# Kernel optimization log

Hardware: AMD Instinct MI355X
Metric: run time of the kernel (lower is better)

## Reference

```python
import jax, jax.numpy as jnp
import numpy as np

B, N, C = 4, 1024, 768
H = 12
HD = C // H  # 64
SCALE = HD ** -0.5


def setup_inputs() -> dict:
    key = jax.random.key(0)
    ks = jax.random.split(key, 8)
    s = lambda fan: 1.0 / np.sqrt(fan)
    return {
        "inputs": jax.random.normal(ks[0], (B, N, C), jnp.float32),
        "w_qkv": jax.random.normal(ks[1], (C, 3 * C), jnp.float32) * s(C),
        "w_l": jax.random.normal(ks[2], (H, H), jnp.float32) * s(H),
        "b_l": jnp.zeros((H,), jnp.float32),
        "w_w": jax.random.normal(ks[3], (H, H), jnp.float32) * s(H),
        "b_w": jnp.zeros((H,), jnp.float32),
        "w_proj": jax.random.normal(ks[4], (C, C), jnp.float32) * s(C),
        "b_proj": jnp.zeros((C,), jnp.float32),
    }


def reference(inputs, w_qkv, w_l, b_l, w_w, b_w, w_proj, b_proj):
    b, n, c = inputs.shape
    qkv = inputs @ w_qkv                      # (B,N,3C), no bias (use_att_bias=False)
    qkv = qkv.reshape(b, n, 3, H, HD)
    qkv = jnp.transpose(qkv, (2, 0, 3, 1, 4))  # (3,B,H,N,HD)
    q = qkv[0] * SCALE
    k = qkv[1]
    v = qkv[2]
    att = jnp.einsum("bhqd,bhkd->bhqk", q, k)            # (B,H,N,N)
    # pre-softmax talking-heads mix over head axis
    att = jnp.einsum("bhqk,hg->bgqk", att, w_l) + b_l[None, :, None, None]
    att = jax.nn.softmax(att, axis=-1)
    # post-softmax talking-heads mix
    att = jnp.einsum("bhqk,hg->bgqk", att, w_w) + b_w[None, :, None, None]
    x = jnp.einsum("bhqk,bhkd->bqhd", att, v).reshape(b, n, c)
    return x @ w_proj + b_proj
```

## Files before the change

kernel.cpp:

```cpp
#include <hip/hip_runtime.h>


#define Bsz   4
#define Nseq  1024
#define Cdim  768
#define Hn    12
#define HDim  64

typedef __attribute__((ext_vector_type(4))) float    f32x4;
typedef __attribute__((ext_vector_type(2))) float    f32x2;
typedef __attribute__((ext_vector_type(8))) _Float16 f16x8;
typedef __attribute__((ext_vector_type(4))) _Float16 f16x4;

#define MFMA_F16(A, B, C) __builtin_amdgcn_mfma_f32_16x16x32_f16(A, B, C, 0, 0, 0)

__global__ __launch_bounds__(256) void cvt_f32_f16(
    const float* __restrict__ in, _Float16* __restrict__ out)
{
  const size_t i = (size_t)(blockIdx.x * 256 + threadIdx.x) * 4;
  float4 v = *(const float4*)(in + i);
  f16x4 o;
  o[0] = (_Float16)v.x; o[1] = (_Float16)v.y;
  o[2] = (_Float16)v.z; o[3] = (_Float16)v.w;
  *(f16x4*)(out + i) = o;
}

__global__ __launch_bounds__(256) void transpose_cvt(
    const float* __restrict__ in, _Float16* __restrict__ out, int R, int C)
{
  __shared__ float T[64][65];
  const int c0 = blockIdx.x * 64, r0 = blockIdx.y * 64;
  const int lr = threadIdx.x >> 4, lc = (threadIdx.x & 15) * 4;
#pragma unroll
  for (int i = 0; i < 4; ++i) {
    float4 v = *(const float4*)(in + (size_t)(r0 + lr + i*16) * C + c0 + lc);
    T[lr+i*16][lc+0] = v.x; T[lr+i*16][lc+1] = v.y;
    T[lr+i*16][lc+2] = v.z; T[lr+i*16][lc+3] = v.w;
  }
  __syncthreads();
#pragma unroll
  for (int i = 0; i < 4; ++i) {
    const int orow = lr + i*16;
    f16x4 o;
#pragma unroll
    for (int j = 0; j < 4; ++j) o[j] = (_Float16)T[lc+j][orow];
    *(f16x4*)(out + (size_t)(c0 + orow) * R + r0 + lc) = o;
  }
}

__global__ __launch_bounds__(256, 2) void gemm_f16(
    const _Float16* __restrict__ A, const _Float16* __restrict__ Bt,
    const float* __restrict__ bias, _Float16* __restrict__ C16,
    float* __restrict__ C32, int M, int N, int K)
{
  __shared__ _Float16 sA[2][4][512];
  __shared__ _Float16 sB[2][4][512];
  const int tid = threadIdx.x;
  const int w = tid >> 6, lane = tid & 63;
  const int m0 = blockIdx.y * 128, n0 = blockIdx.x * 128;
  const int frow = lane & 15, fk8 = lane >> 4;

  f32x4 acc[4][4];
#pragma unroll
  for (int i = 0; i < 4; ++i)
#pragma unroll
    for (int j = 0; j < 4; ++j) acc[i][j] = (f32x4)0.f;

  const _Float16* gsrc = (w < 2)
      ? A  + (size_t)(m0 + w*64 + frow) * K + fk8 * 8
      : Bt + (size_t)(n0 + (w - 2)*64 + frow) * K + fk8 * 8;

  for (int kt = 0; kt < K; kt += 32) {
    f16x8 st[4];
#pragma unroll
    for (int j = 0; j < 4; ++j)
      st[j] = *(const f16x8*)(gsrc + kt + (size_t)j * 16 * K);
    __syncthreads();
    if (w < 2) {
#pragma unroll
      for (int j = 0; j < 4; ++j) *(f16x8*)&sA[w][j][lane*8] = st[j];
    } else {
#pragma unroll
      for (int j = 0; j < 4; ++j) *(f16x8*)&sB[w-2][j][lane*8] = st[j];
    }
    __syncthreads();
    f16x8 af[4], bf[4];
#pragma unroll
    for (int mi = 0; mi < 4; ++mi) af[mi] = *(const f16x8*)&sA[w & 1][mi][lane*8];
#pragma unroll
    for (int ni = 0; ni < 4; ++ni) bf[ni] = *(const f16x8*)&sB[w >> 1][ni][lane*8];
#pragma unroll
    for (int mi = 0; mi < 4; ++mi)
#pragma unroll
      for (int ni = 0; ni < 4; ++ni)
        acc[mi][ni] = MFMA_F16(af[mi], bf[ni], acc[mi][ni]);
  }

  const int m0w = m0 + (w & 1) * 64, n0w = n0 + (w >> 1) * 64;
#pragma unroll
  for (int mi = 0; mi < 4; ++mi)
#pragma unroll
    for (int ni = 0; ni < 4; ++ni) {
      const int n = n0w + ni*16 + (lane & 15);
#pragma unroll
      for (int r = 0; r < 4; ++r) {
        const int m = m0w + mi*16 + (lane >> 4)*4 + r;
        if (C16) C16[(size_t)m * N + n] = (_Float16)acc[mi][ni][r];
        else     C32[(size_t)m * N + n] = acc[mi][ni][r] + bias[n];
      }
    }
}

__global__ __launch_bounds__(256, 2) void gemm_s16(
    const _Float16* __restrict__ qkv16, _Float16* __restrict__ S)
{
  __shared__ _Float16 sA[2][4][512];
  __shared__ _Float16 sB[2][4][512];
  const int tid = threadIdx.x;
  const int w = tid >> 6, lane = tid & 63;
  const int m0 = blockIdx.y * 128, n0 = blockIdx.x * 128;
  const int frow = lane & 15, fk8 = lane >> 4;
  const int bh = blockIdx.z;
  const int b = bh / Hn, h = bh % Hn;

  const _Float16* Abase = qkv16 + (size_t)(b * Nseq) * (3*Cdim) + h * HDim;
  const _Float16* Bbase = Abase + Cdim;

  f32x4 acc[4][4];
#pragma unroll
  for (int i = 0; i < 4; ++i)
#pragma unroll
    for (int j = 0; j < 4; ++j) acc[i][j] = (f32x4)0.f;

  const _Float16* gsrc = (w < 2)
      ? Abase + (size_t)(m0 + w*64 + frow) * (3*Cdim) + fk8 * 8
      : Bbase + (size_t)(n0 + (w - 2)*64 + frow) * (3*Cdim) + fk8 * 8;

#pragma unroll
  for (int kt = 0; kt < HDim; kt += 32) {
    f16x8 st[4];
#pragma unroll
    for (int j = 0; j < 4; ++j)
      st[j] = *(const f16x8*)(gsrc + kt + (size_t)j * 16 * (3*Cdim));
    __syncthreads();
    if (w < 2) {
#pragma unroll
      for (int j = 0; j < 4; ++j) *(f16x8*)&sA[w][j][lane*8] = st[j];
    } else {
#pragma unroll
      for (int j = 0; j < 4; ++j) *(f16x8*)&sB[w-2][j][lane*8] = st[j];
    }
    __syncthreads();
    f16x8 af[4], bf[4];
#pragma unroll
    for (int mi = 0; mi < 4; ++mi) af[mi] = *(const f16x8*)&sA[w & 1][mi][lane*8];
#pragma unroll
    for (int ni = 0; ni < 4; ++ni) bf[ni] = *(const f16x8*)&sB[w >> 1][ni][lane*8];
#pragma unroll
    for (int mi = 0; mi < 4; ++mi)
#pragma unroll
      for (int ni = 0; ni < 4; ++ni)
        acc[mi][ni] = MFMA_F16(af[mi], bf[ni], acc[mi][ni]);
  }

  _Float16* out = S + ((size_t)bh << 20);
  const int m0w = m0 + (w & 1) * 64, n0w = n0 + (w >> 1) * 64;
#pragma unroll
  for (int mi = 0; mi < 4; ++mi)
#pragma unroll
    for (int ni = 0; ni < 4; ++ni) {
      const int n = n0w + ni*16 + (lane & 15);
#pragma unroll
      for (int r = 0; r < 4; ++r) {
        const int m = m0w + mi*16 + (lane >> 4)*4 + r;
        out[(size_t)m * Nseq + n] = (_Float16)acc[mi][ni][r];
      }
    }
}

__global__ __launch_bounds__(256) void mixexp2_k(
    _Float16* __restrict__ S, const float* __restrict__ w_l,
    const float* __restrict__ w_w, const float* __restrict__ b_w)
{
  __shared__ __attribute__((aligned(16))) float wl_s[144];
  __shared__ __attribute__((aligned(16))) float ww_s[144];
  __shared__ float bw_s[12];
  const int tid = threadIdx.x;
  if (tid < 144) { wl_s[tid] = w_l[tid] * 0.125f; ww_s[tid] = w_w[tid]; }
  if (tid < 12)  bw_s[tid] = b_w[tid];
  __syncthreads();

  const int b    = blockIdx.x >> 8;
  const int qg   = blockIdx.x & 255;
  const int w    = tid >> 6;
  const int lane = tid & 63;
  const int q    = qg * 4 + w;
  const int ks   = lane * 16;
  _Float16* base = S + ((size_t)(b*Hn) << 20) + ((size_t)q << 10) + ks;

  f16x8 sv[12][2];
#pragma unroll
  for (int h = 0; h < 12; ++h) {
    sv[h][0] = *(const f16x8*)(base + ((size_t)h << 20));
    sv[h][1] = *(const f16x8*)(base + ((size_t)h << 20) + 8);
  }

  float dacc[12];
#pragma unroll
  for (int g = 0; g < 12; ++g) dacc[g] = 0.f;

#pragma unroll
  for (int bl = 0; bl < 2; ++bl) {
#pragma unroll
    for (int kp = 0; kp < 4; ++kp) {
      const int k0 = kp * 2;
      f32x2 L[12];
#pragma unroll
      for (int g = 0; g < 12; ++g) L[g] = (f32x2)0.f;
#pragma unroll
      for (int h = 0; h < 12; ++h) {
        f32x2 s2;
        s2.x = (float)sv[h][bl][k0];
        s2.y = (float)sv[h][bl][k0+1];
#pragma unroll
        for (int g = 0; g < 12; ++g)
          L[g] += s2 * wl_s[h*12 + g];
      }
#pragma unroll
      for (int g = 0; g < 12; ++g) {
        const _Float16 p0 = (_Float16)__expf(L[g].x - 6.0f);
        const _Float16 p1 = (_Float16)__expf(L[g].y - 6.0f);
        sv[g][bl][k0]   = p0;
        sv[g][bl][k0+1] = p1;
        dacc[g] += (float)p0 + (float)p1;
      }
    }
  }

#pragma unroll
  for (int g = 0; g < 12; ++g) {
    float v = dacc[g];
    v += __shfl_xor(v, 1, 64);
    v += __shfl_xor(v, 2, 64);
    v += __shfl_xor(v, 4, 64);
    v += __shfl_xor(v, 8, 64);
    v += __shfl_xor(v, 16, 64);
    v += __shfl_xor(v, 32, 64);
    dacc[g] = 1.0f / v;
  }

#pragma unroll
  for (int bl = 0; bl < 2; ++bl) {
#pragma unroll
    for (int kp = 0; kp < 4; ++kp) {
      const int k0 = kp * 2;
      f32x2 pr[12];
#pragma unroll
      for (int g = 0; g < 12; ++g) {
        f32x2 t;
        t.x = (float)sv[g][bl][k0];
        t.y = (float)sv[g][bl][k0+1];
        pr[g] = t * dacc[g];
      }
      f32x2 att[12];
#pragma unroll
      for (int g2 = 0; g2 < 12; ++g2) att[g2] = (f32x2)bw_s[g2];
#pragma unroll
      for (int g = 0; g < 12; ++g) {
#pragma unroll
        for (int g2 = 0; g2 < 12; ++g2)
          att[g2] += pr[g] * ww_s[g*12 + g2];
      }
#pragma unroll
      for (int g2 = 0; g2 < 12; ++g2) {
        sv[g2][bl][k0]   = (_Float16)att[g2].x;
        sv[g2][bl][k0+1] = (_Float16)att[g2].y;
      }
    }
  }

#pragma unroll
  for (int g2 = 0; g2 < 12; ++g2) {
    *(f16x8*)(base + ((size_t)g2 << 20))     = sv[g2][0];
    *(f16x8*)(base + ((size_t)g2 << 20) + 8) = sv[g2][1];
  }
}

__global__ __launch_bounds__(256) void prep_v(
    const _Float16* __restrict__ qkv16, _Float16* __restrict__ Vt)
{
  __shared__ float vt[64][65];
  const int id = blockIdx.x;
  const int nt = id & 15;
  const int h  = (id >> 4) % Hn;
  const int b  = id / (16 * Hn);
  const int n0 = nt * 64;
  const int tid = threadIdx.x;
  const int row = tid >> 2;
  const int c0  = (tid & 3) * 16;

  const _Float16* src = qkv16 + (size_t)(b*Nseq + n0 + row) * (3*Cdim) + 2*Cdim + h*HDim + c0;
  f16x8 v0 = *(const f16x8*)src;
  f16x8 v1 = *(const f16x8*)(src + 8);
#pragma unroll
  for (int j = 0; j < 8; ++j) {
    vt[c0+j][row]   = (float)v0[j];
    vt[c0+8+j][row] = (float)v1[j];
  }
  __syncthreads();
  f16x8 o0, o1;
#pragma unroll
  for (int j = 0; j < 8; ++j) {
    o0[j] = (_Float16)vt[row][c0+j];
    o1[j] = (_Float16)vt[row][c0+8+j];
  }
  _Float16* dst = Vt + (size_t)((b*Hn + h)*HDim + row) * Nseq + n0 + c0;
  *(f16x8*)dst = o0;
  *(f16x8*)(dst + 8) = o1;
}

__global__ __launch_bounds__(256, 2) void gemm_pv(
    const _Float16* __restrict__ P, const _Float16* __restrict__ Vt,
    _Float16* __restrict__ x16)
{
  __shared__ _Float16 sA[2][4][512];
  __shared__ _Float16 sB[4][512];
  const int tid = threadIdx.x;
  const int w = tid >> 6, lane = tid & 63;
  const int m0 = blockIdx.y * 128;
  const int bh = blockIdx.z;
  const int b = bh / Hn, g2 = bh % Hn;
  const int frow = lane & 15, fk8 = lane >> 4;

  const _Float16* Abase = P + ((size_t)bh << 20);
  const _Float16* Bbase = Vt + (size_t)(bh * HDim) * Nseq;

  f32x4 acc[4][2];
#pragma unroll
  for (int i = 0; i < 4; ++i)
#pragma unroll
    for (int j = 0; j < 2; ++j) acc[i][j] = (f32x4)0.f;

  const _Float16* gsrc = (w < 2)
      ? Abase + (size_t)(m0 + w*64 + frow) * Nseq + fk8 * 8
      : Bbase + (size_t)frow * Nseq + fk8 * 8;

  for (int kt = 0; kt < Nseq; kt += 32) {
    f16x8 st[4];
    if (w <= 2) {
#pragma unroll
      for (int j = 0; j < 4; ++j)
        st[j] = *(const f16x8*)(gsrc + kt + (size_t)j * 16 * Nseq);
    }
    __syncthreads();
    if (w < 2) {
#pragma unroll
      for (int j = 0; j < 4; ++j) *(f16x8*)&sA[w][j][lane*8] = st[j];
    } else if (w == 2) {
#pragma unroll
      for (int j = 0; j < 4; ++j) *(f16x8*)&sB[j][lane*8] = st[j];
    }
    __syncthreads();
    f16x8 af[4], bf[2];
#pragma unroll
    for (int mi = 0; mi < 4; ++mi) af[mi] = *(const f16x8*)&sA[w & 1][mi][lane*8];
#pragma unroll
    for (int ni = 0; ni < 2; ++ni) bf[ni] = *(const f16x8*)&sB[(w >> 1)*2 + ni][lane*8];
#pragma unroll
    for (int mi = 0; mi < 4; ++mi)
#pragma unroll
      for (int ni = 0; ni < 2; ++ni)
        acc[mi][ni] = MFMA_F16(af[mi], bf[ni], acc[mi][ni]);
  }

  const int m0w = m0 + (w & 1) * 64, n0w = (w >> 1) * 32;
#pragma unroll
  for (int mi = 0; mi < 4; ++mi)
#pragma unroll
    for (int ni = 0; ni < 2; ++ni) {
      const int n = n0w + ni*16 + (lane & 15);
#pragma unroll
      for (int r = 0; r < 4; ++r) {
        const int m = m0w + mi*16 + (lane >> 4)*4 + r;
        x16[(size_t)(b*Nseq + m) * Cdim + g2*HDim + n] = (_Float16)acc[mi][ni][r];
      }
    }
}

__global__ __launch_bounds__(256, 2) void dsum_k(
    const _Float16* __restrict__ qkv16, const float* __restrict__ w_l,
    float* __restrict__ dpart)
{
  __shared__ __attribute__((aligned(16))) float wl_s[144];
  __shared__ float dred[4][16][12];
  const int tid = threadIdx.x;
  const int w = tid >> 6, lane = tid & 63;
  const int col = lane & 15, grp = lane >> 4;
  const int ch = blockIdx.x & 7;
  const int qt = (blockIdx.x >> 3) & 63;
  const int b  = blockIdx.x >> 9;
  const int q0 = qt << 4;

  if (tid < 144) wl_s[tid] = w_l[tid] * 0.125f;

  f16x8 qf[12][2];
  {
    const _Float16* qrow = qkv16 + (size_t)(b*Nseq + q0 + col) * (3*Cdim) + grp*8;
#pragma unroll
    for (int h = 0; h < 12; ++h) {
      qf[h][0] = *(const f16x8*)(qrow + h*HDim);
      qf[h][1] = *(const f16x8*)(qrow + h*HDim + 32);
    }
  }
  __syncthreads();

  float dacc[4][12];
#pragma unroll
  for (int r = 0; r < 4; ++r)
#pragma unroll
    for (int g = 0; g < 12; ++g) dacc[r][g] = 0.f;

#pragma unroll
  for (int kg = 0; kg < 2; ++kg) {
    const int key = ch*128 + kg*64 + w*16 + col;
    const _Float16* krow = qkv16 + (size_t)(b*Nseq + key) * (3*Cdim) + Cdim + grp*8;
    f32x4 S[12];
#pragma unroll
    for (int h = 0; h < 12; ++h) {
      f16x8 b0 = *(const f16x8*)(krow + h*HDim);
      f16x8 b1 = *(const f16x8*)(krow + h*HDim + 32);
      f32x4 s = (f32x4)0.f;
      s = MFMA_F16(qf[h][0], b0, s);
      S[h] = MFMA_F16(qf[h][1], b1, s);
    }
#pragma unroll
    for (int r = 0; r < 4; ++r) {
      float L[12];
#pragma unroll
      for (int g = 0; g < 12; ++g) L[g] = 0.f;
#pragma unroll
      for (int h = 0; h < 12; ++h) {
        const float s = S[h][r];
        const f32x4 w0 = *(const f32x4*)&wl_s[h*12];
        const f32x4 w1 = *(const f32x4*)&wl_s[h*12+4];
        const f32x4 w2 = *(const f32x4*)&wl_s[h*12+8];
#pragma unroll
        for (int j = 0; j < 4; ++j) {
          L[j]   = fmaf(s, w0[j], L[j]);
          L[4+j] = fmaf(s, w1[j], L[4+j]);
          L[8+j] = fmaf(s, w2[j], L[8+j]);
        }
      }
#pragma unroll
      for (int g = 0; g < 12; ++g) dacc[r][g] += __expf(L[g] - 6.0f);
    }
  }
#pragma unroll
  for (int r = 0; r < 4; ++r)
#pragma unroll
    for (int g = 0; g < 12; ++g) {
      float v = dacc[r][g];
      v += __shfl_xor(v, 1, 64);
      v += __shfl_xor(v, 2, 64);
      v += __shfl_xor(v, 4, 64);
      v += __shfl_xor(v, 8, 64);
      dacc[r][g] = v;
    }
  if (col == 0) {
#pragma unroll
    for (int r = 0; r < 4; ++r)
#pragma unroll
      for (int g = 0; g < 12; ++g) dred[w][grp*4+r][g] = dacc[r][g];
  }
  __syncthreads();
  if (tid < 192) {
    const int q = tid / 12, g = tid % 12;
    const float s = dred[0][q][g] + dred[1][q][g] + dred[2][q][g] + dred[3][q][g];
    dpart[((size_t)((b*Hn + g)*Nseq) + q0 + q) * 8 + ch] = s;
  }
}

__global__ __launch_bounds__(256) void dinv_k(
    const float* __restrict__ dpart, float* __restrict__ dinv)
{
  const int i = blockIdx.x * 256 + threadIdx.x;
  const float* p = dpart + (size_t)i * 8;
  f32x4 a = *(const f32x4*)p;
  f32x4 c = *(const f32x4*)(p + 4);
  dinv[i] = 1.0f / (a[0]+a[1]+a[2]+a[3]+c[0]+c[1]+c[2]+c[3]);
}

__global__ __launch_bounds__(256, 2) void pvmix_k(
    const _Float16* __restrict__ qkv16, const _Float16* __restrict__ Vt,
    const float* __restrict__ dinv,
    const float* __restrict__ w_l, const float* __restrict__ w_w,
    const float* __restrict__ b_w, float* __restrict__ x32)
{
  __shared__ _Float16 P_s[12][16][72];
  __shared__ float dinv_s[16][12];
  __shared__ __attribute__((aligned(16))) float wl_s[144];
  __shared__ __attribute__((aligned(16))) float ww_s[144];
  __shared__ float bw_s[12];

  const int tid = threadIdx.x;
  const int w = tid >> 6, lane = tid & 63;
  const int col = lane & 15, grp = lane >> 4;
  const int kh = blockIdx.x & 1;
  const int qt = (blockIdx.x >> 1) & 63;
  const int b  = blockIdx.x >> 7;
  const int q0 = qt << 4;

  if (tid < 144) { wl_s[tid] = w_l[tid] * 0.125f; ww_s[tid] = w_w[tid]; }
  if (tid < 12)  bw_s[tid] = b_w[tid];
  if (tid < 192) {
    const int q = tid / 12, g = tid % 12;
    dinv_s[q][g] = dinv[(size_t)((b*Hn + g)*Nseq) + q0 + q];
  }

  f16x8 qf[12][2];
  {
    const _Float16* qrow = qkv16 + (size_t)(b*Nseq + q0 + col) * (3*Cdim) + grp*8;
#pragma unroll
    for (int h = 0; h < 12; ++h) {
      qf[h][0] = *(const f16x8*)(qrow + h*HDim);
      qf[h][1] = *(const f16x8*)(qrow + h*HDim + 32);
    }
  }
  __syncthreads();

  f32x4 Y[12];
#pragma unroll
  for (int g2 = 0; g2 < 12; ++g2) Y[g2] = (f32x4)0.f;

  for (int c = kh*8; c < kh*8 + 8; ++c) {
    const int k0 = c * 64;
    const _Float16* krow = qkv16 + (size_t)(b*Nseq + k0 + w*16 + col) * (3*Cdim)
                           + Cdim + grp*8;
    f32x4 S[12];
#pragma unroll
    for (int h = 0; h < 12; ++h) {
      f16x8 b0 = *(const f16x8*)(krow + h*HDim);
      f16x8 b1 = *(const f16x8*)(krow + h*HDim + 32);
      f32x4 s = (f32x4)0.f;
      s = MFMA_F16(qf[h][0], b0, s);
      S[h] = MFMA_F16(qf[h][1], b1, s);
    }
    __syncthreads();
#pragma unroll
    for (int r = 0; r < 4; ++r) {
      const int q = grp*4 + r;
      float L[12];
#pragma unroll
      for (int g = 0; g < 12; ++g) L[g] = 0.f;
#pragma unroll
      for (int h = 0; h < 12; ++h) {
        const float s = S[h][r];
        const f32x4 w0 = *(const f32x4*)&wl_s[h*12];
        const f32x4 w1 = *(const f32x4*)&wl_s[h*12+4];
        const f32x4 w2 = *(const f32x4*)&wl_s[h*12+8];
#pragma unroll
        for (int j = 0; j < 4; ++j) {
          L[j]   = fmaf(s, w0[j], L[j]);
          L[4+j] = fmaf(s, w1[j], L[4+j]);
          L[8+j] = fmaf(s, w2[j], L[8+j]);
        }
      }
      float att2[12];
#pragma unroll
      for (int g2 = 0; g2 < 12; ++g2) att2[g2] = bw_s[g2];
#pragma unroll
      for (int g = 0; g < 12; ++g) {
        const float pr = __expf(L[g] - 6.0f) * dinv_s[q][g];
        const f32x4 w0 = *(const f32x4*)&ww_s[g*12];
        const f32x4 w1 = *(const f32x4*)&ww_s[g*12+4];
        const f32x4 w2 = *(const f32x4*)&ww_s[g*12+8];
#pragma unroll
        for (int j = 0; j < 4; ++j) {
          att2[j]   = fmaf(pr, w0[j], att2[j]);
          att2[4+j] = fmaf(pr, w1[j], att2[4+j]);
          att2[8+j] = fmaf(pr, w2[j], att2[8+j]);
        }
      }
#pragma unroll
      for (int g2 = 0; g2 < 12; ++g2)
        P_s[g2][q][w*16 + col] = (_Float16)att2[g2];
    }
    __syncthreads();
#pragma unroll
    for (int g2 = 0; g2 < 12; ++g2) {
      f16x8 a0 = *(const f16x8*)&P_s[g2][col][grp*8];
      f16x8 a1 = *(const f16x8*)&P_s[g2][col][32 + grp*8];
      const _Float16* vb = Vt + (size_t)((b*Hn + g2)*HDim + w*16 + col) * Nseq
                           + k0 + grp*8;
      f16x8 v0 = *(const f16x8*)vb;
      f16x8 v1 = *(const f16x8*)(vb + 32);
      Y[g2] = MFMA_F16(a0, v0, Y[g2]);
      Y[g2] = MFMA_F16(a1, v1, Y[g2]);
    }
  }

#pragma unroll
  for (int g2 = 0; g2 < 12; ++g2)
#pragma unroll
    for (int r = 0; r < 4; ++r)
      atomicAdd(&x32[(size_t)(b*Nseq + q0 + grp*4 + r) * Cdim + g2*HDim + w*16 + col],
                Y[g2][r]);
}

extern "C" void kernel_launch(void* const* d_in, const int* in_sizes, int n_in,
                              void* d_out, int out_size, void* d_ws, size_t ws_size,
                              hipStream_t stream) {
  (void)in_sizes; (void)n_in; (void)out_size;
  const float* inputs = (const float*)d_in[0];
  const float* w_qkv  = (const float*)d_in[1];
  const float* w_l    = (const float*)d_in[2];
  const float* w_w    = (const float*)d_in[4];
  const float* b_w    = (const float*)d_in[5];
  const float* w_proj = (const float*)d_in[6];
  const float* b_proj = (const float*)d_in[7];
  float* out = (float*)d_out;

  const int M = Bsz * Nseq;
  char* ws = (char*)d_ws;
  _Float16* A16   = (_Float16*)ws;
  _Float16* BtQKV = A16   + (size_t)M * Cdim;
  _Float16* BtPrj = BtQKV + (size_t)(3*Cdim) * Cdim;
  _Float16* qkv16 = BtPrj + (size_t)Cdim * Cdim;
  _Float16* Vt    = qkv16 + (size_t)M * 3 * Cdim;
  _Float16* x16   = Vt    + (size_t)M * Cdim;
  float*    dpart = (float*)(x16 + (size_t)M * Cdim);
  float*    dinv  = dpart + (size_t)Bsz*Hn*Nseq*8;
  float*    x32   = dinv  + (size_t)Bsz*Hn*Nseq;
  _Float16* S     = (_Float16*)(x32 + (size_t)M * Cdim);

  const size_t NEED = 42467328ull + 14352384ull + 100663296ull;

  cvt_f32_f16<<<dim3((M * Cdim) / 1024), 256, 0, stream>>>(inputs, A16);
  transpose_cvt<<<dim3((3*Cdim)/64, Cdim/64), 256, 0, stream>>>(w_qkv, BtQKV, Cdim, 3*Cdim);
  transpose_cvt<<<dim3(Cdim/64, Cdim/64), 256, 0, stream>>>(w_proj, BtPrj, Cdim, Cdim);

  gemm_f16<<<dim3((3*Cdim)/128, M/128), 256, 0, stream>>>(
      A16, BtQKV, nullptr, qkv16, nullptr, M, 3*Cdim, Cdim);

  prep_v<<<dim3(Bsz*Hn*16), 256, 0, stream>>>(qkv16, Vt);

  if (ws_size >= NEED) {
    gemm_s16<<<dim3(Nseq/128, Nseq/128, Bsz*Hn), 256, 0, stream>>>(qkv16, S);
    mixexp2_k<<<dim3(Bsz*Nseq/4), 256, 0, stream>>>(S, w_l, w_w, b_w);
    gemm_pv<<<dim3(1, Nseq/128, Bsz*Hn), 256, 0, stream>>>(S, Vt, x16);
  } else {
    dsum_k<<<dim3(Bsz*64*8), 256, 0, stream>>>(qkv16, w_l, dpart);
    dinv_k<<<dim3(Bsz*Hn*Nseq/256), 256, 0, stream>>>(dpart, dinv);
    hipMemsetAsync(x32, 0, (size_t)M*Cdim*sizeof(float), stream);
    pvmix_k<<<dim3(Bsz*64*2), 256, 0, stream>>>(
        qkv16, Vt, dinv, w_l, w_w, b_w, x32);
    cvt_f32_f16<<<dim3((M * Cdim) / 1024), 256, 0, stream>>>(x32, x16);
  }

  gemm_f16<<<dim3(Cdim/128, M/128), 256, 0, stream>>>(
      x16, BtPrj, b_proj, nullptr, out, M, Cdim, Cdim);
}
```

Measured before the change: 291.7 us.

## Halve P·V tile height and coalesce mixexp2 key-column loads

In the talking-heads softmax kernel, each lane now reads two 8-element chunks spaced 512 apart instead of 16 contiguous elements, so neighbouring lanes touch adjacent 16-byte segments and global accesses coalesce better. Each half is stored as soon as it is finished rather than all at the end. The P·V GEMM tile shrinks from 128 to 64 rows, doubling the grid to 768 blocks for better CU occupancy. All four waves now share the global-to-LDS loading instead of three. The smaller tile reads Vt twice as often in exchange for more parallelism.

```diff
diff --git a/kernel.cpp b/kernel.cpp
--- a/kernel.cpp
+++ b/kernel.cpp
@@ -195,14 +195,14 @@
   const int w    = tid >> 6;
   const int lane = tid & 63;
   const int q    = qg * 4 + w;
-  const int ks   = lane * 16;
-  _Float16* base = S + ((size_t)(b*Hn) << 20) + ((size_t)q << 10) + ks;
+  _Float16* base0 = S + ((size_t)(b*Hn) << 20) + ((size_t)q << 10) + lane*8;
+  _Float16* base1 = base0 + 512;
 
   f16x8 sv[12][2];
 #pragma unroll
   for (int h = 0; h < 12; ++h) {
-    sv[h][0] = *(const f16x8*)(base + ((size_t)h << 20));
-    sv[h][1] = *(const f16x8*)(base + ((size_t)h << 20) + 8);
+    sv[h][0] = *(const f16x8*)(base0 + ((size_t)h << 20));
+    sv[h][1] = *(const f16x8*)(base1 + ((size_t)h << 20));
   }
 
   float dacc[12];
@@ -277,12 +277,10 @@
         sv[g2][bl][k0+1] = (_Float16)att[g2].y;
       }
     }
-  }
-
-#pragma unroll
-  for (int g2 = 0; g2 < 12; ++g2) {
-    *(f16x8*)(base + ((size_t)g2 << 20))     = sv[g2][0];
-    *(f16x8*)(base + ((size_t)g2 << 20) + 8) = sv[g2][1];
+    _Float16* bb = (bl == 0) ? base0 : base1;
+#pragma unroll
+    for (int g2 = 0; g2 < 12; ++g2)
+      *(f16x8*)(bb + ((size_t)g2 << 20)) = sv[g2][bl];
   }
 }
 
@@ -323,11 +321,11 @@
     const _Float16* __restrict__ P, const _Float16* __restrict__ Vt,
     _Float16* __restrict__ x16)
 {
-  __shared__ _Float16 sA[2][4][512];
+  __shared__ _Float16 sA[4][512];
   __shared__ _Float16 sB[4][512];
   const int tid = threadIdx.x;
   const int w = tid >> 6, lane = tid & 63;
-  const int m0 = blockIdx.y * 128;
+  const int m0 = blockIdx.y * 64;
   const int bh = blockIdx.z;
   const int b = bh / Hn, g2 = bh % Hn;
   const int frow = lane & 15, fk8 = lane >> 4;
@@ -335,47 +333,47 @@
   const _Float16* Abase = P + ((size_t)bh << 20);
   const _Float16* Bbase = Vt + (size_t)(bh * HDim) * Nseq;
 
-  f32x4 acc[4][2];
-#pragma unroll
-  for (int i = 0; i < 4; ++i)
+  f32x4 acc[2][2];
+#pragma unroll
+  for (int i = 0; i < 2; ++i)
 #pragma unroll
     for (int j = 0; j < 2; ++j) acc[i][j] = (f32x4)0.f;
 
   const _Float16* gsrc = (w < 2)
-      ? Abase + (size_t)(m0 + w*64 + frow) * Nseq + fk8 * 8
-      : Bbase + (size_t)frow * Nseq + fk8 * 8;
+      ? Abase + (size_t)(m0 + w*32 + frow) * Nseq + fk8 * 8
+      : Bbase + (size_t)((w - 2)*32 + frow) * Nseq + fk8 * 8;
+
+  const int mw = w & 1, nw = w >> 1;
 
   for (int kt = 0; kt < Nseq; kt += 32) {
-    f16x8 st[4];
-    if (w <= 2) {
-#pragma unroll
-      for (int j = 0; j < 4; ++j)
-        st[j] = *(const f16x8*)(gsrc + kt + (size_t)j * 16 * Nseq);
-    }
+    f16x8 st[2];
+#pragma unroll
+    for (int j = 0; j < 2; ++j)
+      st[j] = *(const f16x8*)(gsrc + kt + (size_t)j * 16 * Nseq);
     __syncthreads();
     if (w < 2) {
 #pragma unroll
-      for (int j = 0; j < 4; ++j) *(f16x8*)&sA[w][j][lane*8] = st[j];
-    } else if (w == 2) {
-#pragma unroll
-      for (int j = 0; j < 4; ++j) *(f16x8*)&sB[j][lane*8] = st[j];
-    }
-    __syncthreads();
-    f16x8 af[4], bf[2];
-#pragma unroll
-    for (int mi = 0; mi < 4; ++mi) af[mi] = *(const f16x8*)&sA[w & 1][mi][lane*8];
-#pragma unroll
-    for (int ni = 0; ni < 2; ++ni) bf[ni] = *(const f16x8*)&sB[(w >> 1)*2 + ni][lane*8];
-#pragma unroll
-    for (int mi = 0; mi < 4; ++mi)
+      for (int j = 0; j < 2; ++j) *(f16x8*)&sA[w*2 + j][lane*8] = st[j];
+    } else {
+#pragma unroll
+      for (int j = 0; j < 2; ++j) *(f16x8*)&sB[(w-2)*2 + j][lane*8] = st[j];
+    }
+    __syncthreads();
+    f16x8 af[2], bf[2];
+#pragma unroll
+    for (int mi = 0; mi < 2; ++mi) af[mi] = *(const f16x8*)&sA[mw*2 + mi][lane*8];
+#pragma unroll
+    for (int ni = 0; ni < 2; ++ni) bf[ni] = *(const f16x8*)&sB[nw*2 + ni][lane*8];
+#pragma unroll
+    for (int mi = 0; mi < 2; ++mi)
 #pragma unroll
       for (int ni = 0; ni < 2; ++ni)
         acc[mi][ni] = MFMA_F16(af[mi], bf[ni], acc[mi][ni]);
   }
 
-  const int m0w = m0 + (w & 1) * 64, n0w = (w >> 1) * 32;
-#pragma unroll
-  for (int mi = 0; mi < 4; ++mi)
+  const int m0w = m0 + mw*32, n0w = nw*32;
+#pragma unroll
+  for (int mi = 0; mi < 2; ++mi)
 #pragma unroll
     for (int ni = 0; ni < 2; ++ni) {
       const int n = n0w + ni*16 + (lane & 15);
@@ -647,7 +645,7 @@
   if (ws_size >= NEED) {
     gemm_s16<<<dim3(Nseq/128, Nseq/128, Bsz*Hn), 256, 0, stream>>>(qkv16, S);
     mixexp2_k<<<dim3(Bsz*Nseq/4), 256, 0, stream>>>(S, w_l, w_w, b_w);
-    gemm_pv<<<dim3(1, Nseq/128, Bsz*Hn), 256, 0, stream>>>(S, Vt, x16);
+    gemm_pv<<<dim3(1, Nseq/64, Bsz*Hn), 256, 0, stream>>>(S, Vt, x16);
   } else {
     dsum_k<<<dim3(Bsz*64*8), 256, 0, stream>>>(qkv16, w_l, dpart);
     dinv_k<<<dim3(Bsz*Hn*Nseq/256), 256, 0, stream>>>(dpart, dinv);
```

After: 309.3 us. 6.1% more time.
